# Kernel tuning notes

Measured on AMD Instinct MI355X. Metric: run time of the kernel, lower is better.

## Reference

```python
import jax, jax.numpy as jnp
import numpy as np
import math

HGT, WID = 24, 24          # shape2d
NUM_HEADS = 12
EMB = 768
HEAD_DIM = EMB // NUM_HEADS
N_GRID = HGT * WID         # 576 spatial tokens
N_TOK = N_GRID + 1         # +1 CLS token
BATCH = 32


def _rel_indices(h: int, w: int) -> np.ndarray:
    """[(h*w), (h*w)] indices into the (2h-1)*(2w-1) relative table."""
    y = np.arange(h)
    x = np.arange(w)
    y1, x1, y2, x2 = np.meshgrid(y, x, y, x, indexing='ij')
    idx = (y1 - y2 + h - 1) * (2 * w - 1) + (x1 - x2 + w - 1)
    return idx.reshape(h * w, h * w)


def setup_inputs() -> dict:
    key = jax.random.key(0)
    ks = jax.random.split(key, 6)
    s = 0.02
    return {
        "x": jax.random.normal(ks[0], (BATCH, N_TOK, EMB), dtype=jnp.float32),
        "Wq": jax.random.normal(ks[1], (EMB, EMB), dtype=jnp.float32) * s,
        "bq": jnp.zeros((EMB,), dtype=jnp.float32),
        "Wk": jax.random.normal(ks[2], (EMB, EMB), dtype=jnp.float32) * s,
        "bk": jnp.zeros((EMB,), dtype=jnp.float32),
        "Wv": jax.random.normal(ks[3], (EMB, EMB), dtype=jnp.float32) * s,
        "bv": jnp.zeros((EMB,), dtype=jnp.float32),
        "Wp": jax.random.normal(ks[4], (EMB, EMB), dtype=jnp.float32) * s,
        "bp": jnp.zeros((EMB,), dtype=jnp.float32),
        "rel_table": jax.random.normal(ks[5], ((2 * HGT - 1) * (2 * WID - 1), NUM_HEADS), dtype=jnp.float32) * s,
    }


def reference(x, Wq, bq, Wk, bk, Wv, bv, Wp, bp, rel_table):
    B, N, E = x.shape
    scale = 1.0 / math.sqrt(HEAD_DIM)

    def heads(t):  # [B,N,E] -> [B,H,N,hd]
        return t.reshape(B, N, NUM_HEADS, HEAD_DIM).transpose(0, 2, 1, 3)

    q = heads(x @ Wq.T + bq)
    k = heads(x @ Wk.T + bk)
    v = heads(x @ Wv.T + bv)

    scores = jnp.einsum('bhqd,bhkd->bhqk', q, k) * scale  # [B,H,N,N]

    # relative position bias on spatial tokens (skip CLS row/col)
    idx = jnp.asarray(_rel_indices(HGT, WID))              # [Ng,Ng]
    bias = rel_table[idx].transpose(2, 0, 1)               # [H,Ng,Ng]
    scores = scores.at[:, :, 1:, 1:].add(bias)

    attn = jax.nn.softmax(scores, axis=-1)
    out = jnp.einsum('bhqk,bhkd->bhqd', attn, v)           # [B,H,N,hd]
    out = out.transpose(0, 2, 1, 3).reshape(B, N, E)
    return out @ Wp.T + bp
```

## Files before the change

kernel.cpp:

```cpp
#include <hip/hip_runtime.h>
#include <hip/hip_bf16.h>
#include <stdint.h>

#define HGT   24
#define WID   24
#define NHEAD 12
#define EMB   768
#define HD    64
#define NGRID 576
#define NTOK  577
#define NPAD  640
#define BATCH 32
#define MROWS (BATCH * NTOK)
#define NKT   10
#define NQT   5
#define QKVC  (3 * EMB)

typedef __attribute__((ext_vector_type(8))) short bf16x8;
typedef __attribute__((ext_vector_type(4))) float f32x4;

__device__ __forceinline__ short f2bf(float f) {
    union { float f; unsigned u; } c; c.f = f;
    unsigned r = (c.u + 0x7FFFu + ((c.u >> 16) & 1u)) >> 16;
    return (short)(r & 0xFFFFu);
}
__device__ __forceinline__ float b2f(short s) {
    union { unsigned u; float f; } c; c.u = ((unsigned)(unsigned short)s) << 16;
    return c.f;
}
__device__ __forceinline__ unsigned pk2bf(float a, float b) {
    __hip_bfloat162 h = __float22bfloat162_rn(make_float2(a, b));
    union { __hip_bfloat162 h; unsigned u; } c; c.h = h;
    return c.u;
}
__device__ __forceinline__ float fexp2(float x) {
#if __has_builtin(__builtin_amdgcn_exp2f)
    return __builtin_amdgcn_exp2f(x);
#else
    return __expf(x * 0.69314718f);
#endif
}

__device__ __forceinline__ void gload16(void* lds, const void* g) {
    __builtin_amdgcn_global_load_lds(
        (const __attribute__((address_space(1))) void*)g,
        (__attribute__((address_space(3))) void*)lds, 16, 0, 0);
}

__device__ __forceinline__ void wait_vm0_barrier() {
    asm volatile("s_waitcnt vmcnt(0)" ::: "memory");
    __builtin_amdgcn_s_barrier();
}

__device__ __forceinline__ int xcd_swizzle(int orig, int nwg) {
    int q = nwg >> 3, r = nwg & 7;
    int xcd = orig & 7, idx = orig >> 3;
    return (xcd < r) ? xcd * (q + 1) + idx : r * (q + 1) + (xcd - r) * q + idx;
}

__global__ void cast_f32_bf16(const float* __restrict__ src, short* __restrict__ dst, int n) {
    int i = (blockIdx.x * blockDim.x + threadIdx.x) * 4;
    int stride = gridDim.x * blockDim.x * 4;
    for (int j = i; j < n; j += stride) {
        float4 v = *(const float4*)(src + j);
        uint2 o;
        o.x = pk2bf(v.x, v.y);
        o.y = pk2bf(v.z, v.w);
        *(uint2*)(dst + j) = o;
    }
}

__global__ void bias_expand(const float* __restrict__ rel, short* __restrict__ be) {
    const float L2E = 1.44269504f;
    int q = blockIdx.x;
    int k = threadIdx.x;
    float v[NHEAD];
    if (k >= NTOK) {
#pragma unroll
        for (int h = 0; h < NHEAD; h++) v[h] = -1e30f;
    } else if (q == 0 || q >= NTOK || k == 0) {
#pragma unroll
        for (int h = 0; h < NHEAD; h++) v[h] = 0.f;
    } else {
        int i = q - 1, j = k - 1;
        int idx = ((i / WID) - (j / WID) + HGT - 1) * (2 * WID - 1)
                + ((i % WID) - (j % WID) + WID - 1);
        const float* rp = rel + (size_t)idx * NHEAD;
#pragma unroll
        for (int h = 0; h < NHEAD; h++) v[h] = rp[h];
    }
#pragma unroll
    for (int h = 0; h < NHEAD; h++)
        be[((size_t)h * NPAD + q) * NPAD + k] = f2bf(v[h] * L2E);
}

__global__ __launch_bounds__(256) void transpose_v(const short* __restrict__ qnat, short* __restrict__ vt) {
    __shared__ __align__(16) short T[64][72];
    int bi = blockIdx.x;
    int kt = bi % NKT;
    int h  = (bi / NKT) % NHEAD;
    int b  = bi / (NKT * NHEAD);
    int t  = threadIdx.x;

    int r  = t >> 2, cb = (t & 3) * 16;
    int key = kt * 64 + r; if (key >= NTOK) key = NTOK - 1;
    const short* src = qnat + (size_t)(b * NTOK + key) * QKVC + 2 * EMB + h * HD;
    *(int4*)&T[r][cb]     = *(const int4*)(src + cb);
    *(int4*)&T[r][cb + 8] = *(const int4*)(src + cb + 8);
    __syncthreads();

    int d = t >> 2, kb = (t & 3) * 16;
    short tmp[16];
#pragma unroll
    for (int s = 0; s < 16; s++) tmp[s] = T[kb + s][d];
    short* dst = vt + (((size_t)b * NHEAD + h) * HD + d) * NPAD + kt * 64 + kb;
    *(int4*)&dst[0] = *(int4*)&tmp[0];
    *(int4*)&dst[8] = *(int4*)&tmp[8];
}

template <int MODE>
__global__ __launch_bounds__(512) void gemm_bt(
    const short* __restrict__ A, const short* __restrict__ Bw,
    const float* __restrict__ b0, const float* __restrict__ b1, const float* __restrict__ b2,
    void* __restrict__ Outp, int M)
{
    constexpr int NC  = (MODE == 0) ? QKVC : EMB;
    constexpr int NBX = NC / 256;
    constexpr int K   = EMB;
    constexpr int NST = K / 32;

    __shared__ __align__(16) short Asl[4][256][32];
    __shared__ __align__(16) short Bsl[4][256][32];

    const int t    = threadIdx.x;
    const int lane = t & 63;
    const int w    = t >> 6;
    const int wm   = w >> 2;
    const int wn   = w & 3;
    const int lg   = lane >> 4;
    const int li   = lane & 15;

    const int nwg  = NBX * ((MROWS + 255) / 256);
    const int wgid = xcd_swizzle(blockIdx.x, nwg);
    const int tm   = (wgid / NBX) * 256;
    const int tn   = (wgid % NBX) * 256;

    const int drow = lane >> 2;
    const int lc   = (lane & 3) ^ ((lane >> 3) & 3);
    const int xsw  = (li >> 1) & 3;

    const short* agp[2];
    const short* bgp[2];
#pragma unroll
    for (int gi = 0; gi < 2; gi++) {
        int rm = tm + gi * 128 + w * 16 + drow; if (rm >= M) rm = M - 1;
        agp[gi] = A  + (size_t)rm * K + lc * 8;
        bgp[gi] = Bw + (size_t)(tn + gi * 128 + w * 16 + drow) * K + lc * 8;
    }

    f32x4 acc[8][4];
#pragma unroll
    for (int i = 0; i < 8; i++)
#pragma unroll
        for (int j = 0; j < 4; j++) acc[i][j] = (f32x4){0.f, 0.f, 0.f, 0.f};

#pragma unroll
    for (int ss = 0; ss < 3; ss++) {
        gload16(&Asl[ss][0 * 128 + w * 16][0], agp[0] + ss * 32);
        gload16(&Asl[ss][1 * 128 + w * 16][0], agp[1] + ss * 32);
        gload16(&Bsl[ss][0 * 128 + w * 16][0], bgp[0] + ss * 32);
        gload16(&Bsl[ss][1 * 128 + w * 16][0], bgp[1] + ss * 32);
    }

    for (int s = 0; s < NST; s++) {
        if (s < NST - 2)       asm volatile("s_waitcnt vmcnt(8)" ::: "memory");
        else if (s == NST - 2) asm volatile("s_waitcnt vmcnt(4)" ::: "memory");
        else                   asm volatile("s_waitcnt vmcnt(0)" ::: "memory");
        __builtin_amdgcn_s_barrier();

        const int cb = s & 3;
        bf16x8 af[8], bfv[4];
#pragma unroll
        for (int mi = 0; mi < 8; mi++)
            af[mi] = *(const bf16x8*)&Asl[cb][wm * 128 + mi * 16 + li][(lg ^ xsw) * 8];
#pragma unroll
        for (int nj = 0; nj < 4; nj++)
            bfv[nj] = *(const bf16x8*)&Bsl[cb][wn * 64 + nj * 16 + li][(lg ^ xsw) * 8];

        if (s + 3 < NST) {
            const int tb = (s + 3) & 3;
            const int ko = (s + 3) * 32;
            gload16(&Asl[tb][0 * 128 + w * 16][0], agp[0] + ko);
            gload16(&Asl[tb][1 * 128 + w * 16][0], agp[1] + ko);
            gload16(&Bsl[tb][0 * 128 + w * 16][0], bgp[0] + ko);
            gload16(&Bsl[tb][1 * 128 + w * 16][0], bgp[1] + ko);
        }

        __builtin_amdgcn_s_setprio(1);
#pragma unroll
        for (int mi = 0; mi < 8; mi++)
#pragma unroll
            for (int nj = 0; nj < 4; nj++)
                acc[mi][nj] = __builtin_amdgcn_mfma_f32_16x16x32_bf16(
                    bfv[nj], af[mi], acc[mi][nj], 0, 0, 0);
        __builtin_amdgcn_s_setprio(0);
    }

#pragma unroll
    for (int nj = 0; nj < 4; nj++) {
        const int ccb = tn + wn * 64 + nj * 16 + lg * 4;
        float4 bias4;
        if constexpr (MODE == 0) {
            int which = (ccb >= 2 * EMB) ? 2 : ((ccb >= EMB) ? 1 : 0);
            const float* bb = (which == 0) ? b0 : ((which == 1) ? b1 : b2);
            bias4 = *(const float4*)&bb[ccb - which * EMB];
        } else {
            bias4 = *(const float4*)&b0[ccb];
        }
#pragma unroll
        for (int mi = 0; mi < 8; mi++) {
            int m = tm + wm * 128 + mi * 16 + li;
            if (m >= M) continue;
            if constexpr (MODE == 0) {
                uint2 o;
                o.x = pk2bf(acc[mi][nj][0] + bias4.x, acc[mi][nj][1] + bias4.y);
                o.y = pk2bf(acc[mi][nj][2] + bias4.z, acc[mi][nj][3] + bias4.w);
                *(uint2*)&((short*)Outp)[(size_t)m * NC + ccb] = o;
            } else {
                float4 o;
                o.x = acc[mi][nj][0] + bias4.x;
                o.y = acc[mi][nj][1] + bias4.y;
                o.z = acc[mi][nj][2] + bias4.z;
                o.w = acc[mi][nj][3] + bias4.w;
                *(float4*)&((float*)Outp)[(size_t)m * NC + ccb] = o;
            }
        }
    }
}

__global__ __launch_bounds__(512) void attn_kernel(
    const short* __restrict__ qnat, const short* __restrict__ vt,
    const short* __restrict__ biasx, short* __restrict__ aout)
{
    __shared__ __align__(16) short Ksl[2][64][64];
    __shared__ __align__(16) short Vsl[2][64][64];
    __shared__ __align__(16) short Psl[8][16][64];

    const int wg = (blockIdx.x & 7) * (BATCH * NHEAD * NQT / 8) + (blockIdx.x >> 3);
    const int qt = wg % NQT;
    const int rest = wg / NQT;
    const int b  = rest & 31;
    const int h  = rest >> 5;

    const int t    = threadIdx.x;
    const int lane = t & 63;
    const int w    = t >> 6;
    const int lg   = lane >> 4;
    const int li   = lane & 15;
    const int xh   = li & 7;
    const int qbase = qt * 128;
    const int myq  = qbase + w * 16 + li;

    const float SCL = 0.18033688f;

    const short* qp  = qnat + (size_t)b * NTOK * QKVC + h * HD;
    const short* kp  = qp + EMB;
    const short* vtp = vt + ((size_t)b * NHEAD + h) * (size_t)HD * NPAD;
    const short* browq = biasx + ((size_t)h * NPAD + myq) * NPAD;

    bf16x8 qf[2];
    {
        int qrow = myq < NTOK ? myq : NTOK - 1;
        qf[0] = *(const bf16x8*)(qp + (size_t)qrow * QKVC + lg * 8);
        qf[1] = *(const bf16x8*)(qp + (size_t)qrow * QKVC + 32 + lg * 8);
    }

    float mrun = -1e30f, lrun = 0.f;
    f32x4 oacc[4];
#pragma unroll
    for (int d = 0; d < 4; d++) oacc[d] = (f32x4){0.f, 0.f, 0.f, 0.f};

    const int srow = w * 8 + (lane >> 3);
    const int cofs = ((lane & 7) ^ (lane >> 3)) * 8;

    {
        int key = srow; if (key >= NTOK) key = NTOK - 1;
        gload16(&Ksl[0][w * 8][0], kp + (size_t)key * QKVC + cofs);
        gload16(&Vsl[0][w * 8][0], vtp + (size_t)srow * NPAD + cofs);
    }
    short4 bcur[4];
#pragma unroll
    for (int j = 0; j < 4; j++) bcur[j] = *(const short4*)&browq[j * 16 + lg * 4];
    wait_vm0_barrier();

    short (*Kc)[64] = Ksl[0], (*Kn)[64] = Ksl[1];
    short (*Vc)[64] = Vsl[0], (*Vn)[64] = Vsl[1];

    for (int kt = 0; kt < NKT; kt++) {
        if (kt + 1 < NKT) {
            int key = (kt + 1) * 64 + srow; if (key >= NTOK) key = NTOK - 1;
            gload16(&Kn[w * 8][0], kp + (size_t)key * QKVC + cofs);
            gload16(&Vn[w * 8][0], vtp + (size_t)srow * NPAD + (kt + 1) * 64 + cofs);
        }
        short4 bnxt[4];
        {
            int ktn = (kt + 1 < NKT) ? kt + 1 : kt;
#pragma unroll
            for (int j = 0; j < 4; j++)
                bnxt[j] = *(const short4*)&browq[ktn * 64 + j * 16 + lg * 4];
        }

        float pvv[4][4];
        __builtin_amdgcn_s_setprio(1);
#pragma unroll
        for (int j = 0; j < 4; j++) {
            bf16x8 ak0 = *(const bf16x8*)&Kc[j * 16 + li][(lg ^ xh) * 8];
            bf16x8 ak1 = *(const bf16x8*)&Kc[j * 16 + li][((4 + lg) ^ xh) * 8];
            f32x4 s = (f32x4){0.f, 0.f, 0.f, 0.f};
            s = __builtin_amdgcn_mfma_f32_16x16x32_bf16(ak0, qf[0], s, 0, 0, 0);
            s = __builtin_amdgcn_mfma_f32_16x16x32_bf16(ak1, qf[1], s, 0, 0, 0);
            pvv[j][0] = fmaf(s[0], SCL, b2f(bcur[j].x));
            pvv[j][1] = fmaf(s[1], SCL, b2f(bcur[j].y));
            pvv[j][2] = fmaf(s[2], SCL, b2f(bcur[j].z));
            pvv[j][3] = fmaf(s[3], SCL, b2f(bcur[j].w));
        }
        __builtin_amdgcn_s_setprio(0);

        float mt = pvv[0][0];
#pragma unroll
        for (int j = 0; j < 4; j++)
#pragma unroll
            for (int r = 0; r < 4; r++) mt = fmaxf(mt, pvv[j][r]);
        mt = fmaxf(mt, __shfl_xor(mt, 16, 64));
        mt = fmaxf(mt, __shfl_xor(mt, 32, 64));
        if (__any(mt > mrun + 8.0f)) {
            float nm  = fmaxf(mrun, mt);
            float fac = fexp2(mrun - nm);
            mrun = nm;
            lrun *= fac;
#pragma unroll
            for (int d = 0; d < 4; d++) oacc[d] *= fac;
        }
        float rs = 0.f;
#pragma unroll
        for (int j = 0; j < 4; j++)
#pragma unroll
            for (int r = 0; r < 4; r++) {
                float p = fexp2(pvv[j][r] - mrun);
                pvv[j][r] = p;
                rs += p;
            }
        rs += __shfl_xor(rs, 16, 64);
        rs += __shfl_xor(rs, 32, 64);
        lrun += rs;

#pragma unroll
        for (int j = 0; j < 4; j++) {
            uint2 pw;
            pw.x = pk2bf(pvv[j][0], pvv[j][1]);
            pw.y = pk2bf(pvv[j][2], pvv[j][3]);
            *(uint2*)&Psl[w][li][(((2 * j + (lg >> 1)) ^ xh) * 8) + (lg & 1) * 4] = pw;
        }

        __builtin_amdgcn_s_setprio(1);
#pragma unroll
        for (int dd = 0; dd < 4; dd++) {
#pragma unroll
            for (int kk = 0; kk < 2; kk++) {
                bf16x8 av = *(const bf16x8*)&Vc[dd * 16 + li][((kk * 4 + lg) ^ xh) * 8];
                bf16x8 pb = *(const bf16x8*)&Psl[w][li][((kk * 4 + lg) ^ xh) * 8];
                oacc[dd] = __builtin_amdgcn_mfma_f32_16x16x32_bf16(av, pb, oacc[dd], 0, 0, 0);
            }
        }
        __builtin_amdgcn_s_setprio(0);

        wait_vm0_barrier();
        short (*tp)[64];
        tp = Kc; Kc = Kn; Kn = tp;
        tp = Vc; Vc = Vn; Vn = tp;
#pragma unroll
        for (int j = 0; j < 4; j++) bcur[j] = bnxt[j];
    }

    if (myq < NTOK) {
        float inv = 1.0f / lrun;
        short* op = aout + ((size_t)b * NTOK + myq) * EMB + h * HD;
#pragma unroll
        for (int dd = 0; dd < 4; dd++) {
            uint2 o;
            o.x = pk2bf(oacc[dd][0] * inv, oacc[dd][1] * inv);
            o.y = pk2bf(oacc[dd][2] * inv, oacc[dd][3] * inv);
            *(uint2*)&op[dd * 16 + lg * 4] = o;
        }
    }
}

extern "C" void kernel_launch(void* const* d_in, const int* in_sizes, int n_in,
                              void* d_out, int out_size, void* d_ws, size_t ws_size,
                              hipStream_t stream) {
    (void)in_sizes; (void)n_in; (void)out_size; (void)ws_size;
    const float* x   = (const float*)d_in[0];
    const float* Wq  = (const float*)d_in[1];
    const float* bq  = (const float*)d_in[2];
    const float* Wk  = (const float*)d_in[3];
    const float* bk  = (const float*)d_in[4];
    const float* Wv  = (const float*)d_in[5];
    const float* bv  = (const float*)d_in[6];
    const float* Wp  = (const float*)d_in[7];
    const float* bp  = (const float*)d_in[8];
    const float* rel = (const float*)d_in[9];

    const size_t WN = (size_t)EMB * EMB;
    short* Wb   = (short*)d_ws;
    short* Wpb  = Wb + 3 * WN;
    short* qnat = Wpb + WN;
    short* xb   = qnat + (size_t)MROWS * QKVC;
    short* aout = xb;
    short* vtb  = xb + (size_t)MROWS * EMB;
    short* bexp = vtb + (size_t)BATCH * NHEAD * HD * NPAD;

    const int XN = MROWS * EMB;
    const int MT = (MROWS + 255) / 256;
    cast_f32_bf16<<<576, 256, 0, stream>>>(Wq, Wb, (int)WN);
    cast_f32_bf16<<<576, 256, 0, stream>>>(Wk, Wb + WN, (int)WN);
    cast_f32_bf16<<<576, 256, 0, stream>>>(Wv, Wb + 2 * WN, (int)WN);
    cast_f32_bf16<<<576, 256, 0, stream>>>(Wp, Wpb, (int)WN);
    cast_f32_bf16<<<13848, 256, 0, stream>>>(x, xb, XN);
    bias_expand<<<NPAD, NPAD, 0, stream>>>(rel, bexp);

    gemm_bt<0><<<9 * MT, 512, 0, stream>>>(xb, Wb, bq, bk, bv, qnat, MROWS);
    transpose_v<<<BATCH * NHEAD * NKT, 256, 0, stream>>>(qnat, vtb);
    attn_kernel<<<BATCH * NHEAD * NQT, 512, 0, stream>>>(qnat, vtb, bexp, aout);
    gemm_bt<1><<<3 * MT, 512, 0, stream>>>(aout, Wpb, bp, bp, bp, d_out, MROWS);
}
```

Measured before the change: 282.8 us.

## Fuse V transpose into QKV GEMM epilogue and process 128 keys per attention step

The QKV GEMM epilogue now writes V columns directly in transposed [b,h,d,n] layout, removing the separate transpose_v kernel and its extra read and write of V. The attention kernel loads two 64-key tiles per iteration (128 keys), doubling LDS buffers and halving barriers and online-softmax rescale checks per key. The transposed epilogue stores are scalar 2-byte strided writes, which may coalesce poorly, and the larger LDS footprint may reduce occupancy.

```diff
diff --git a/kernel.cpp b/kernel.cpp
--- a/kernel.cpp
+++ b/kernel.cpp
@@ -13,6 +13,7 @@
 #define BATCH 32
 #define MROWS (BATCH * NTOK)
 #define NKT   10
+#define NIT   5
 #define NQT   5
 #define QKVC  (3 * EMB)
 
@@ -94,35 +95,11 @@
         be[((size_t)h * NPAD + q) * NPAD + k] = f2bf(v[h] * L2E);
 }
 
-__global__ __launch_bounds__(256) void transpose_v(const short* __restrict__ qnat, short* __restrict__ vt) {
-    __shared__ __align__(16) short T[64][72];
-    int bi = blockIdx.x;
-    int kt = bi % NKT;
-    int h  = (bi / NKT) % NHEAD;
-    int b  = bi / (NKT * NHEAD);
-    int t  = threadIdx.x;
-
-    int r  = t >> 2, cb = (t & 3) * 16;
-    int key = kt * 64 + r; if (key >= NTOK) key = NTOK - 1;
-    const short* src = qnat + (size_t)(b * NTOK + key) * QKVC + 2 * EMB + h * HD;
-    *(int4*)&T[r][cb]     = *(const int4*)(src + cb);
-    *(int4*)&T[r][cb + 8] = *(const int4*)(src + cb + 8);
-    __syncthreads();
-
-    int d = t >> 2, kb = (t & 3) * 16;
-    short tmp[16];
-#pragma unroll
-    for (int s = 0; s < 16; s++) tmp[s] = T[kb + s][d];
-    short* dst = vt + (((size_t)b * NHEAD + h) * HD + d) * NPAD + kt * 64 + kb;
-    *(int4*)&dst[0] = *(int4*)&tmp[0];
-    *(int4*)&dst[8] = *(int4*)&tmp[8];
-}
-
 template <int MODE>
 __global__ __launch_bounds__(512) void gemm_bt(
     const short* __restrict__ A, const short* __restrict__ Bw,
     const float* __restrict__ b0, const float* __restrict__ b1, const float* __restrict__ b2,
-    void* __restrict__ Outp, int M)
+    void* __restrict__ Outp, short* __restrict__ vout, int M)
 {
     constexpr int NC  = (MODE == 0) ? QKVC : EMB;
     constexpr int NBX = NC / 256;
@@ -206,33 +183,55 @@
         __builtin_amdgcn_s_setprio(0);
     }
 
-#pragma unroll
-    for (int nj = 0; nj < 4; nj++) {
-        const int ccb = tn + wn * 64 + nj * 16 + lg * 4;
-        float4 bias4;
-        if constexpr (MODE == 0) {
-            int which = (ccb >= 2 * EMB) ? 2 : ((ccb >= EMB) ? 1 : 0);
-            const float* bb = (which == 0) ? b0 : ((which == 1) ? b1 : b2);
-            bias4 = *(const float4*)&bb[ccb - which * EMB];
-        } else {
-            bias4 = *(const float4*)&b0[ccb];
-        }
-#pragma unroll
-        for (int mi = 0; mi < 8; mi++) {
-            int m = tm + wm * 128 + mi * 16 + li;
-            if (m >= M) continue;
+    if (MODE == 0 && tn >= 2 * EMB) {
+#pragma unroll
+        for (int nj = 0; nj < 4; nj++) {
+            const int ccb = tn + wn * 64 + nj * 16 + lg * 4;
+            const int e   = ccb - 2 * EMB;
+            const int hh  = e >> 6, db = e & 63;
+            const float4 bias4 = *(const float4*)&b2[e];
+#pragma unroll
+            for (int mi = 0; mi < 8; mi++) {
+                int m = tm + wm * 128 + mi * 16 + li;
+                if (m >= M) continue;
+                int bi = m / NTOK;
+                int n  = m - bi * NTOK;
+                short* vr = vout + (((size_t)bi * NHEAD + hh) * HD + db) * NPAD + n;
+                vr[0 * NPAD] = f2bf(acc[mi][nj][0] + bias4.x);
+                vr[1 * NPAD] = f2bf(acc[mi][nj][1] + bias4.y);
+                vr[2 * NPAD] = f2bf(acc[mi][nj][2] + bias4.z);
+                vr[3 * NPAD] = f2bf(acc[mi][nj][3] + bias4.w);
+            }
+        }
+    } else {
+#pragma unroll
+        for (int nj = 0; nj < 4; nj++) {
+            const int ccb = tn + wn * 64 + nj * 16 + lg * 4;
+            float4 bias4;
             if constexpr (MODE == 0) {
-                uint2 o;
-                o.x = pk2bf(acc[mi][nj][0] + bias4.x, acc[mi][nj][1] + bias4.y);
-                o.y = pk2bf(acc[mi][nj][2] + bias4.z, acc[mi][nj][3] + bias4.w);
-                *(uint2*)&((short*)Outp)[(size_t)m * NC + ccb] = o;
+                int which = (ccb >= EMB) ? 1 : 0;
+                const float* bb = (which == 0) ? b0 : b1;
+                bias4 = *(const float4*)&bb[ccb - which * EMB];
             } else {
-                float4 o;
-                o.x = acc[mi][nj][0] + bias4.x;
-                o.y = acc[mi][nj][1] + bias4.y;
-                o.z = acc[mi][nj][2] + bias4.z;
-                o.w = acc[mi][nj][3] + bias4.w;
-                *(float4*)&((float*)Outp)[(size_t)m * NC + ccb] = o;
+                bias4 = *(const float4*)&b0[ccb];
+            }
+#pragma unroll
+            for (int mi = 0; mi < 8; mi++) {
+                int m = tm + wm * 128 + mi * 16 + li;
+                if (m >= M) continue;
+                if constexpr (MODE == 0) {
+                    uint2 o;
+                    o.x = pk2bf(acc[mi][nj][0] + bias4.x, acc[mi][nj][1] + bias4.y);
+                    o.y = pk2bf(acc[mi][nj][2] + bias4.z, acc[mi][nj][3] + bias4.w);
+                    *(uint2*)&((short*)Outp)[(size_t)m * NC + ccb] = o;
+                } else {
+                    float4 o;
+                    o.x = acc[mi][nj][0] + bias4.x;
+                    o.y = acc[mi][nj][1] + bias4.y;
+                    o.z = acc[mi][nj][2] + bias4.z;
+                    o.w = acc[mi][nj][3] + bias4.w;
+                    *(float4*)&((float*)Outp)[(size_t)m * NC + ccb] = o;
+                }
             }
         }
     }
@@ -242,8 +241,8 @@
     const short* __restrict__ qnat, const short* __restrict__ vt,
     const short* __restrict__ biasx, short* __restrict__ aout)
 {
-    __shared__ __align__(16) short Ksl[2][64][64];
-    __shared__ __align__(16) short Vsl[2][64][64];
+    __shared__ __align__(16) short Ksl[2][2][64][64];
+    __shared__ __align__(16) short Vsl[2][2][64][64];
     __shared__ __align__(16) short Psl[8][16][64];
 
     const int wg = (blockIdx.x & 7) * (BATCH * NHEAD * NQT / 8) + (blockIdx.x >> 3);
@@ -283,54 +282,68 @@
     const int srow = w * 8 + (lane >> 3);
     const int cofs = ((lane & 7) ^ (lane >> 3)) * 8;
 
-    {
-        int key = srow; if (key >= NTOK) key = NTOK - 1;
-        gload16(&Ksl[0][w * 8][0], kp + (size_t)key * QKVC + cofs);
-        gload16(&Vsl[0][w * 8][0], vtp + (size_t)srow * NPAD + cofs);
-    }
-    short4 bcur[4];
-#pragma unroll
-    for (int j = 0; j < 4; j++) bcur[j] = *(const short4*)&browq[j * 16 + lg * 4];
+#pragma unroll
+    for (int st = 0; st < 2; st++) {
+        int key = st * 64 + srow; if (key >= NTOK) key = NTOK - 1;
+        gload16(&Ksl[0][st][w * 8][0], kp + (size_t)key * QKVC + cofs);
+        gload16(&Vsl[0][st][w * 8][0], vtp + (size_t)srow * NPAD + st * 64 + cofs);
+    }
+    short4 bcur[2][4];
+#pragma unroll
+    for (int st = 0; st < 2; st++)
+#pragma unroll
+        for (int j = 0; j < 4; j++)
+            bcur[st][j] = *(const short4*)&browq[st * 64 + j * 16 + lg * 4];
     wait_vm0_barrier();
 
-    short (*Kc)[64] = Ksl[0], (*Kn)[64] = Ksl[1];
-    short (*Vc)[64] = Vsl[0], (*Vn)[64] = Vsl[1];
-
-    for (int kt = 0; kt < NKT; kt++) {
-        if (kt + 1 < NKT) {
-            int key = (kt + 1) * 64 + srow; if (key >= NTOK) key = NTOK - 1;
-            gload16(&Kn[w * 8][0], kp + (size_t)key * QKVC + cofs);
-            gload16(&Vn[w * 8][0], vtp + (size_t)srow * NPAD + (kt + 1) * 64 + cofs);
-        }
-        short4 bnxt[4];
+    for (int it = 0; it < NIT; it++) {
+        const int cb = it & 1, nb = cb ^ 1;
+
+        if (it + 1 < NIT) {
+#pragma unroll
+            for (int st = 0; st < 2; st++) {
+                int key = (it + 1) * 128 + st * 64 + srow; if (key >= NTOK) key = NTOK - 1;
+                gload16(&Ksl[nb][st][w * 8][0], kp + (size_t)key * QKVC + cofs);
+                gload16(&Vsl[nb][st][w * 8][0],
+                        vtp + (size_t)srow * NPAD + (it + 1) * 128 + st * 64 + cofs);
+            }
+        }
+        short4 bnxt[2][4];
         {
-            int ktn = (kt + 1 < NKT) ? kt + 1 : kt;
+            int itn = (it + 1 < NIT) ? it + 1 : it;
+#pragma unroll
+            for (int st = 0; st < 2; st++)
+#pragma unroll
+                for (int j = 0; j < 4; j++)
+                    bnxt[st][j] = *(const short4*)&browq[(itn * 2 + st) * 64 + j * 16 + lg * 4];
+        }
+
+        float pvv[2][4][4];
+        __builtin_amdgcn_s_setprio(1);
+#pragma unroll
+        for (int st = 0; st < 2; st++) {
+#pragma unroll
+            for (int j = 0; j < 4; j++) {
+                bf16x8 ak0 = *(const bf16x8*)&Ksl[cb][st][j * 16 + li][(lg ^ xh) * 8];
+                bf16x8 ak1 = *(const bf16x8*)&Ksl[cb][st][j * 16 + li][((4 + lg) ^ xh) * 8];
+                f32x4 s = (f32x4){0.f, 0.f, 0.f, 0.f};
+                s = __builtin_amdgcn_mfma_f32_16x16x32_bf16(ak0, qf[0], s, 0, 0, 0);
+                s = __builtin_amdgcn_mfma_f32_16x16x32_bf16(ak1, qf[1], s, 0, 0, 0);
+                pvv[st][j][0] = fmaf(s[0], SCL, b2f(bcur[st][j].x));
+                pvv[st][j][1] = fmaf(s[1], SCL, b2f(bcur[st][j].y));
+                pvv[st][j][2] = fmaf(s[2], SCL, b2f(bcur[st][j].z));
+                pvv[st][j][3] = fmaf(s[3], SCL, b2f(bcur[st][j].w));
+            }
+        }
+        __builtin_amdgcn_s_setprio(0);
+
+        float mt = pvv[0][0][0];
+#pragma unroll
+        for (int st = 0; st < 2; st++)
 #pragma unroll
             for (int j = 0; j < 4; j++)
-                bnxt[j] = *(const short4*)&browq[ktn * 64 + j * 16 + lg * 4];
-        }
-
-        float pvv[4][4];
-        __builtin_amdgcn_s_setprio(1);
-#pragma unroll
-        for (int j = 0; j < 4; j++) {
-            bf16x8 ak0 = *(const bf16x8*)&Kc[j * 16 + li][(lg ^ xh) * 8];
-            bf16x8 ak1 = *(const bf16x8*)&Kc[j * 16 + li][((4 + lg) ^ xh) * 8];
-            f32x4 s = (f32x4){0.f, 0.f, 0.f, 0.f};
-            s = __builtin_amdgcn_mfma_f32_16x16x32_bf16(ak0, qf[0], s, 0, 0, 0);
-            s = __builtin_amdgcn_mfma_f32_16x16x32_bf16(ak1, qf[1], s, 0, 0, 0);
-            pvv[j][0] = fmaf(s[0], SCL, b2f(bcur[j].x));
-            pvv[j][1] = fmaf(s[1], SCL, b2f(bcur[j].y));
-            pvv[j][2] = fmaf(s[2], SCL, b2f(bcur[j].z));
-            pvv[j][3] = fmaf(s[3], SCL, b2f(bcur[j].w));
-        }
-        __builtin_amdgcn_s_setprio(0);
-
-        float mt = pvv[0][0];
-#pragma unroll
-        for (int j = 0; j < 4; j++)
-#pragma unroll
-            for (int r = 0; r < 4; r++) mt = fmaxf(mt, pvv[j][r]);
+#pragma unroll
+                for (int r = 0; r < 4; r++) mt = fmaxf(mt, pvv[st][j][r]);
         mt = fmaxf(mt, __shfl_xor(mt, 16, 64));
         mt = fmaxf(mt, __shfl_xor(mt, 32, 64));
         if (__any(mt > mrun + 8.0f)) {
@@ -343,43 +356,46 @@
         }
         float rs = 0.f;
 #pragma unroll
-        for (int j = 0; j < 4; j++)
-#pragma unroll
-            for (int r = 0; r < 4; r++) {
-                float p = fexp2(pvv[j][r] - mrun);
-                pvv[j][r] = p;
-                rs += p;
-            }
+        for (int st = 0; st < 2; st++)
+#pragma unroll
+            for (int j = 0; j < 4; j++)
+#pragma unroll
+                for (int r = 0; r < 4; r++) {
+                    float p = fexp2(pvv[st][j][r] - mrun);
+                    pvv[st][j][r] = p;
+                    rs += p;
+                }
         rs += __shfl_xor(rs, 16, 64);
         rs += __shfl_xor(rs, 32, 64);
         lrun += rs;
 
 #pragma unroll
-        for (int j = 0; j < 4; j++) {
-            uint2 pw;
-            pw.x = pk2bf(pvv[j][0], pvv[j][1]);
-            pw.y = pk2bf(pvv[j][2], pvv[j][3]);
-            *(uint2*)&Psl[w][li][(((2 * j + (lg >> 1)) ^ xh) * 8) + (lg & 1) * 4] = pw;
-        }
-
-        __builtin_amdgcn_s_setprio(1);
-#pragma unroll
-        for (int dd = 0; dd < 4; dd++) {
-#pragma unroll
-            for (int kk = 0; kk < 2; kk++) {
-                bf16x8 av = *(const bf16x8*)&Vc[dd * 16 + li][((kk * 4 + lg) ^ xh) * 8];
-                bf16x8 pb = *(const bf16x8*)&Psl[w][li][((kk * 4 + lg) ^ xh) * 8];
-                oacc[dd] = __builtin_amdgcn_mfma_f32_16x16x32_bf16(av, pb, oacc[dd], 0, 0, 0);
-            }
-        }
-        __builtin_amdgcn_s_setprio(0);
+        for (int st = 0; st < 2; st++) {
+#pragma unroll
+            for (int j = 0; j < 4; j++) {
+                uint2 pw;
+                pw.x = pk2bf(pvv[st][j][0], pvv[st][j][1]);
+                pw.y = pk2bf(pvv[st][j][2], pvv[st][j][3]);
+                *(uint2*)&Psl[w][li][(((2 * j + (lg >> 1)) ^ xh) * 8) + (lg & 1) * 4] = pw;
+            }
+            __builtin_amdgcn_s_setprio(1);
+#pragma unroll
+            for (int dd = 0; dd < 4; dd++) {
+#pragma unroll
+                for (int kk = 0; kk < 2; kk++) {
+                    bf16x8 av = *(const bf16x8*)&Vsl[cb][st][dd * 16 + li][((kk * 4 + lg) ^ xh) * 8];
+                    bf16x8 pb = *(const bf16x8*)&Psl[w][li][((kk * 4 + lg) ^ xh) * 8];
+                    oacc[dd] = __builtin_amdgcn_mfma_f32_16x16x32_bf16(av, pb, oacc[dd], 0, 0, 0);
+                }
+            }
+            __builtin_amdgcn_s_setprio(0);
+        }
 
         wait_vm0_barrier();
-        short (*tp)[64];
-        tp = Kc; Kc = Kn; Kn = tp;
-        tp = Vc; Vc = Vn; Vn = tp;
-#pragma unroll
-        for (int j = 0; j < 4; j++) bcur[j] = bnxt[j];
+#pragma unroll
+        for (int st = 0; st < 2; st++)
+#pragma unroll
+            for (int j = 0; j < 4; j++) bcur[st][j] = bnxt[st][j];
     }
 
     if (myq < NTOK) {
@@ -428,8 +444,7 @@
     cast_f32_bf16<<<13848, 256, 0, stream>>>(x, xb, XN);
     bias_expand<<<NPAD, NPAD, 0, stream>>>(rel, bexp);
 
-    gemm_bt<0><<<9 * MT, 512, 0, stream>>>(xb, Wb, bq, bk, bv, qnat, MROWS);
-    transpose_v<<<BATCH * NHEAD * NKT, 256, 0, stream>>>(qnat, vtb);
+    gemm_bt<0><<<9 * MT, 512, 0, stream>>>(xb, Wb, bq, bk, bv, qnat, vtb, MROWS);
     attn_kernel<<<BATCH * NHEAD * NQT, 512, 0, stream>>>(qnat, vtb, bexp, aout);
-    gemm_bt<1><<<3 * MT, 512, 0, stream>>>(aout, Wpb, bp, bp, bp, d_out, MROWS);
-}
+    gemm_bt<1><<<3 * MT, 512, 0, stream>>>(aout, Wpb, bp, bp, bp, d_out, nullptr, MROWS);
+}
```

Result: faster. 265.7 us (-6.1%).
